# Performance work log

Measured on AMD Instinct MI355X. Metric: run time of the kernel, lower is better.

Reference implementation:

```python
import jax, jax.numpy as jnp
import numpy as np

E, B, D, T = 8, 4096, 2048, 2048
H = D // 2 + T // 2  # expert hidden dim = 2048
TOP_K = 2


def setup_inputs() -> dict:
    key = jax.random.key(0)
    ks = jax.random.split(key, 5)
    s_in = 1.0 / np.sqrt(D)
    s_h = 1.0 / np.sqrt(H)
    return {
        "xs": jax.random.normal(ks[0], (E, B, D), dtype=jnp.float32),
        "Wg": jax.random.normal(ks[1], (D,), dtype=jnp.float32) * s_in,
        "bg": jnp.zeros((1,), dtype=jnp.float32),
        "W1": jax.random.normal(ks[2], (E, D, H), dtype=jnp.float32) * s_in,
        "b1": jnp.zeros((E, H), dtype=jnp.float32),
        "W2": jax.random.normal(ks[3], (E, H, T), dtype=jnp.float32) * s_h,
        "b2": jnp.zeros((E, T), dtype=jnp.float32),
    }


def reference(xs, Wg, bg, W1, b1, W2, b2):
    # Gating: logits[b, e] = x[e][b] @ Wg + bg  -> [B, E]
    logits = jnp.einsum("ebd,d->be", xs, Wg) + bg
    probs = jax.nn.softmax(logits, axis=1)
    top_k_values, top_k_indices = jax.lax.top_k(probs, TOP_K)  # [B, K]

    # Dense expert compute over each expert's own input stream.
    # hidden[e, b, h] = relu(x[e] @ W1[e] + b1[e]); out[e, b, t] = hidden @ W2[e] + b2[e]
    hidden = jax.nn.relu(jnp.einsum("ebd,edh->ebh", xs, W1) + b1[:, None, :])
    expert_out = jnp.einsum("ebh,eht->ebt", hidden, W2) + b2[:, None, :]  # [E, B, T]

    # Gather the top-k experts per token. In the original, masked-dense compute
    # + output mask is mathematically identical to this gather.
    per_token = jnp.transpose(expert_out, (1, 0, 2))  # [B, E, T]
    selected = jnp.take_along_axis(per_token, top_k_indices[:, :, None], axis=1)  # [B, K, T]

    out = jnp.sum(top_k_values[:, :, None] * selected, axis=1)  # [B, T]
    return out, top_k_values
```

## Files before the change

### kernel.cpp

```cpp
#include <hip/hip_runtime.h>
#include <hip/hip_bf16.h>
#include <stdint.h>

#define E_ 8
#define B_ 4096
#define D_ 2048
#define T_ 2048
#define H_ 2048
#define KDIM 2048
#define NDIM 2048

typedef __attribute__((ext_vector_type(4))) float f32x4;
typedef __attribute__((ext_vector_type(4))) unsigned short u16x4;
typedef __attribute__((ext_vector_type(8))) unsigned short u16x8;
typedef __attribute__((ext_vector_type(8))) __bf16 bf16x8;

__device__ __forceinline__ unsigned short f2bf(float f) {
    __hip_bfloat16 h = __float2bfloat16(f);
    return __builtin_bit_cast(unsigned short, h);
}

__device__ __forceinline__ void gload_lds16(const void* g, void* lds) {
    __builtin_amdgcn_global_load_lds(
        (const __attribute__((address_space(1))) void*)g,
        (__attribute__((address_space(3))) void*)lds, 16, 0, 0);
}

__global__ __launch_bounds__(256) void moe_gating(
    const float* __restrict__ xs, const float* __restrict__ Wg,
    const float* __restrict__ bg, float* __restrict__ out_topk,
    float* __restrict__ prob_slot, int* __restrict__ counts,
    int* __restrict__ slot_of, unsigned short* __restrict__ A1)
{
    const int b = blockIdx.x;
    const int t = threadIdx.x;
    const int wave = t >> 6, lane = t & 63;
    __shared__ float red[E_][4];
    __shared__ int sh_i0, sh_i1;

    const f32x4 wg0 = ((const f32x4*)Wg)[t];
    const f32x4 wg1 = ((const f32x4*)Wg)[t + 256];

    f32x4 xa[E_], xb[E_];
    #pragma unroll
    for (int e = 0; e < E_; ++e) {
        const f32x4* xr = (const f32x4*)(xs + ((size_t)e * B_ + b) * D_);
        xa[e] = __builtin_nontemporal_load(&xr[t]);
        xb[e] = __builtin_nontemporal_load(&xr[t + 256]);
        float p = xa[e].x*wg0.x + xa[e].y*wg0.y + xa[e].z*wg0.z + xa[e].w*wg0.w
                + xb[e].x*wg1.x + xb[e].y*wg1.y + xb[e].z*wg1.z + xb[e].w*wg1.w;
        #pragma unroll
        for (int off = 32; off >= 1; off >>= 1) p += __shfl_xor(p, off);
        if (lane == 0) red[e][wave] = p;
    }
    __syncthreads();
    if (t == 0) {
        float pr[E_];
        float mx = -3.0e38f;
        #pragma unroll
        for (int e = 0; e < E_; ++e) {
            pr[e] = red[e][0] + red[e][1] + red[e][2] + red[e][3] + bg[0];
            mx = fmaxf(mx, pr[e]);
        }
        float s = 0.f;
        #pragma unroll
        for (int e = 0; e < E_; ++e) { pr[e] = expf(pr[e] - mx); s += pr[e]; }
        float inv = 1.0f / s;
        #pragma unroll
        for (int e = 0; e < E_; ++e) pr[e] *= inv;
        int i0 = 0;
        #pragma unroll
        for (int e = 1; e < E_; ++e) if (pr[e] > pr[i0]) i0 = e;
        int i1 = (i0 == 0) ? 1 : 0;
        #pragma unroll
        for (int e = 0; e < E_; ++e) { if (e != i0 && pr[e] > pr[i1]) i1 = e; }
        float p0 = pr[i0], p1 = pr[i1];
        out_topk[2*b]    = p0;
        out_topk[2*b+1]  = p1;
        prob_slot[2*b]   = p0;
        prob_slot[2*b+1] = p1;
        int pos0 = atomicAdd(&counts[i0], 1);
        slot_of[i0 * B_ + pos0] = 2*b;
        int pos1 = atomicAdd(&counts[i1], 1);
        slot_of[i1 * B_ + pos1] = 2*b + 1;
        sh_i0 = i0; sh_i1 = i1;
    }
    __syncthreads();
    const int i0 = sh_i0, i1 = sh_i1;
    f32x4 s0a = xa[0], s0b = xb[0], s1a = xa[0], s1b = xb[0];
    #pragma unroll
    for (int e = 0; e < E_; ++e) {
        if (i0 == e) { s0a = xa[e]; s0b = xb[e]; }
        if (i1 == e) { s1a = xa[e]; s1b = xb[e]; }
    }
    u16x4 w;
    w[0]=f2bf(s0a.x); w[1]=f2bf(s0a.y); w[2]=f2bf(s0a.z); w[3]=f2bf(s0a.w);
    ((u16x4*)(A1 + (size_t)(2*b) * D_))[t] = w;
    w[0]=f2bf(s0b.x); w[1]=f2bf(s0b.y); w[2]=f2bf(s0b.z); w[3]=f2bf(s0b.w);
    ((u16x4*)(A1 + (size_t)(2*b) * D_ + 1024))[t] = w;
    w[0]=f2bf(s1a.x); w[1]=f2bf(s1a.y); w[2]=f2bf(s1a.z); w[3]=f2bf(s1a.w);
    ((u16x4*)(A1 + (size_t)(2*b+1) * D_))[t] = w;
    w[0]=f2bf(s1b.x); w[1]=f2bf(s1b.y); w[2]=f2bf(s1b.z); w[3]=f2bf(s1b.w);
    ((u16x4*)(A1 + (size_t)(2*b+1) * D_ + 1024))[t] = w;
}

__global__ void build_tiles(const int* __restrict__ counts, int* __restrict__ tiles)
{
    if (threadIdx.x == 0 && blockIdx.x == 0) {
        int n = 0;
        for (int e = 0; e < E_; ++e) {
            int te = (counts[e] + 255) >> 8;
            for (int m = 0; m < te; ++m) tiles[1 + n++] = (e << 16) | m;
        }
        tiles[0] = n;
    }
}

template<int DUAL>
__global__ __launch_bounds__(256) void wtrans(
    const float* __restrict__ Wa, const float* __restrict__ Wb,
    unsigned short* __restrict__ Wta, unsigned short* __restrict__ Wtb)
{
    const int z  = blockIdx.z;
    const int e  = DUAL ? (z & 7) : z;
    const float* W = (DUAL && (z >> 3)) ? Wb : Wa;
    unsigned short* Wt = (DUAL && (z >> 3)) ? Wtb : Wta;
    const int kb = blockIdx.x * 64;
    const int nb = blockIdx.y * 64;
    const int t  = threadIdx.x;
    __shared__ float tile[64][68];

    const float* src = W + ((size_t)e * KDIM + kb) * NDIM + nb;
    {
        const int kr = t >> 2, nc = (t & 3) * 16;
        #pragma unroll
        for (int j = 0; j < 4; ++j) {
            f32x4 v = __builtin_nontemporal_load(
                (const f32x4*)(src + (size_t)kr * NDIM + nc + j * 4));
            *(f32x4*)&tile[kr][nc + j * 4] = v;
        }
    }
    __syncthreads();
    {
        const int nn = t >> 2, kc = (t & 3) * 16;
        unsigned short wbuf[16];
        #pragma unroll
        for (int j = 0; j < 16; ++j) wbuf[j] = f2bf(tile[kc + j][nn]);
        unsigned short* dst = Wt + ((size_t)e * NDIM + nb + nn) * KDIM + kb + kc;
        *(u16x8*)dst       = *(const u16x8*)&wbuf[0];
        *((u16x8*)dst + 1) = *(const u16x8*)&wbuf[8];
    }
}

#define BAR  __builtin_amdgcn_s_barrier()
#define PRIO1 __builtin_amdgcn_s_setprio(1)
#define PRIO0 __builtin_amdgcn_s_setprio(0)

template<int LAYER>
__global__ __launch_bounds__(1024, 4) void moe_gemm(
    const unsigned short* __restrict__ Abuf,
    const unsigned short* __restrict__ Wt,
    const float* __restrict__ bias,
    const int* __restrict__ counts,
    const int* __restrict__ tiles,
    const int* __restrict__ slot_of,
    const float* __restrict__ prob_slot,
    unsigned short* __restrict__ hidden_out,
    float* __restrict__ out)
{
    const int nMt = tiles[0];
    const int bid = blockIdx.x;
    const int mt  = bid >> 3;
    const int np  = bid & 7;
    if (mt >= nMt) return;
    const int info = tiles[1 + mt];
    const int e   = info >> 16;
    const int m0  = (info & 0xffff) * 256;
    const int n0  = np * 256;
    const int n_e = counts[e];

    const int t = threadIdx.x;
    const int lane = t & 63;
    const int w = t >> 6;
    const int wm = (w >> 2) * 64;
    const int wn = (w & 3) * 64;
    const int lg = lane >> 4;

    __shared__ u16x8 As[4 * 1024];
    __shared__ u16x8 Bs[4 * 1024];
    __shared__ int   slots_s[256];
    __shared__ float probs_s[256];

    if (t < 256) {
        int gm = m0 + t;
        int s = -1; float p = 0.f;
        if (gm < n_e) { s = slot_of[e * B_ + gm]; p = prob_slot[s]; }
        slots_s[t] = s; probs_s[t] = p;
    }
    __syncthreads();

    const int ksw = (((t & 3) ^ ((t >> 3) & 3)) << 3);
    const unsigned short* aptr;
    const unsigned short* bptr;
    {
        const int r = t >> 2;
        int s = slots_s[r]; if (s < 0) s = 0;
        aptr = Abuf + (size_t)s * KDIM + ksw;
        bptr = Wt + ((size_t)e * NDIM + n0 + r) * KDIM + ksw;
    }

#define STGA(BUF, KT) gload_lds16(aptr + (KT)*32, &As[(BUF)*1024 + w*64])
#define STGB(BUF, KT) gload_lds16(bptr + (KT)*32, &Bs[(BUF)*1024 + w*64])

    f32x4 acc[4][4];
    #pragma unroll
    for (int i = 0; i < 4; ++i)
        #pragma unroll
        for (int j = 0; j < 4; ++j) {
            f32x4 z = {0.f, 0.f, 0.f, 0.f};
            acc[i][j] = z;
        }

    STGA(0, 0); STGB(0, 0);
    STGA(1, 1); STGB(1, 1);
    STGA(2, 2); STGB(2, 2);

    const int usw = (lane >> 1) & 3;
    for (int kt = 0; kt < 64; ++kt) {
        asm volatile("s_waitcnt vmcnt(4)" ::: "memory");
        BAR;
        int tn = kt + 3; if (tn > 63) tn = 63;
        const int nb = (kt + 3) & 3;
        const int base = (kt & 3) * 1024;

        STGA(nb, tn);
        bf16x8 af[4];
        #pragma unroll
        for (int mi = 0; mi < 4; ++mi) {
            const int row = wm + mi * 16 + (lane & 15);
            af[mi] = __builtin_bit_cast(bf16x8, As[base + row * 4 + (lg ^ usw)]);
        }
        bf16x8 bq0, bq1;
        {
            const int r0 = wn + 0 * 16 + (lane & 15);
            const int r1 = wn + 1 * 16 + (lane & 15);
            bq0 = __builtin_bit_cast(bf16x8, Bs[base + r0 * 4 + (lg ^ usw)]);
            bq1 = __builtin_bit_cast(bf16x8, Bs[base + r1 * 4 + (lg ^ usw)]);
        }
        PRIO1;
        #pragma unroll
        for (int mi = 0; mi < 4; ++mi)
            acc[mi][0] = __builtin_amdgcn_mfma_f32_16x16x32_bf16(af[mi], bq0, acc[mi][0], 0, 0, 0);
        #pragma unroll
        for (int mi = 0; mi < 4; ++mi)
            acc[mi][1] = __builtin_amdgcn_mfma_f32_16x16x32_bf16(af[mi], bq1, acc[mi][1], 0, 0, 0);
        PRIO0;

        STGB(nb, tn);
        bf16x8 bq2, bq3;
        {
            const int r2 = wn + 2 * 16 + (lane & 15);
            const int r3 = wn + 3 * 16 + (lane & 15);
            bq2 = __builtin_bit_cast(bf16x8, Bs[base + r2 * 4 + (lg ^ usw)]);
            bq3 = __builtin_bit_cast(bf16x8, Bs[base + r3 * 4 + (lg ^ usw)]);
        }
        PRIO1;
        #pragma unroll
        for (int mi = 0; mi < 4; ++mi)
            acc[mi][2] = __builtin_amdgcn_mfma_f32_16x16x32_bf16(af[mi], bq2, acc[mi][2], 0, 0, 0);
        #pragma unroll
        for (int mi = 0; mi < 4; ++mi)
            acc[mi][3] = __builtin_amdgcn_mfma_f32_16x16x32_bf16(af[mi], bq3, acc[mi][3], 0, 0, 0);
        PRIO0;
    }
    asm volatile("s_waitcnt vmcnt(0)" ::: "memory");

    #pragma unroll
    for (int mi = 0; mi < 4; ++mi) {
        #pragma unroll
        for (int rr = 0; rr < 4; ++rr) {
            const int rloc = wm + mi * 16 + ((lane >> 4) << 2) + rr;
            const int s = slots_s[rloc];
            if (s < 0) continue;
            #pragma unroll
            for (int ni = 0; ni < 4; ++ni) {
                const int col = n0 + wn + ni * 16 + (lane & 15);
                float v = acc[mi][ni][rr];
                if (LAYER == 1) {
                    v += bias[e * NDIM + col];
                    v = fmaxf(v, 0.f);
                    hidden_out[(size_t)s * H_ + col] = f2bf(v);
                } else {
                    v = (v + bias[e * NDIM + col]) * probs_s[rloc];
                    atomicAdd(&out[(size_t)(s >> 1) * T_ + col], v);
                }
            }
        }
    }
#undef STGA
#undef STGB
}

extern "C" void kernel_launch(void* const* d_in, const int* in_sizes, int n_in,
                              void* d_out, int out_size, void* d_ws, size_t ws_size,
                              hipStream_t stream)
{
    const float* xs = (const float*)d_in[0];
    const float* Wg = (const float*)d_in[1];
    const float* bg = (const float*)d_in[2];
    const float* W1 = (const float*)d_in[3];
    const float* b1 = (const float*)d_in[4];
    const float* W2 = (const float*)d_in[5];
    const float* b2 = (const float*)d_in[6];

    float* out      = (float*)d_out;
    float* out_topk = out + (size_t)B_ * T_;

    char* ws = (char*)d_ws;
    int*   counts    = (int*)ws;
    int*   tiles     = (int*)(ws + 256);
    int*   slot_of   = (int*)(ws + 768);
    float* prob_slot = (float*)(ws + 768 + E_ * B_ * 4);
    size_t off = 768 + (size_t)E_ * B_ * 4 + 2 * B_ * 4;
    off = (off + 255) & ~(size_t)255;
    unsigned short* A1     = (unsigned short*)(ws + off); off += (size_t)2 * B_ * D_ * 2;
    unsigned short* hidden = (unsigned short*)(ws + off); off += (size_t)2 * B_ * H_ * 2;
    unsigned short* Wt1    = (unsigned short*)(ws + off); off += (size_t)E_ * KDIM * NDIM * 2;
    size_t off_big = off + (size_t)E_ * KDIM * NDIM * 2;
    unsigned short* Wt2 = (unsigned short*)(ws + off);

    const bool big = (ws_size >= off_big);

    hipMemsetAsync(counts, 0, 256, stream);
    hipMemsetAsync(out, 0, (size_t)B_ * T_ * sizeof(float), stream);

    dim3 blk(256), gblk(1024);
    dim3 ggrid(39 * 8);

    if (big) {
        dim3 tgrid(32, 32, 16);
        wtrans<1><<<tgrid, blk, 0, stream>>>(W1, W2, Wt1, Wt2);
        moe_gating<<<dim3(B_), dim3(256), 0, stream>>>(
            xs, Wg, bg, out_topk, prob_slot, counts, slot_of, A1);
        build_tiles<<<dim3(1), dim3(64), 0, stream>>>(counts, tiles);
        moe_gemm<1><<<ggrid, gblk, 0, stream>>>(
            A1, Wt1, b1, counts, tiles, slot_of, prob_slot, hidden, nullptr);
        moe_gemm<2><<<ggrid, gblk, 0, stream>>>(
            hidden, Wt2, b2, counts, tiles, slot_of, prob_slot, nullptr, out);
    } else {
        dim3 tgrid(32, 32, E_);
        moe_gating<<<dim3(B_), dim3(256), 0, stream>>>(
            xs, Wg, bg, out_topk, prob_slot, counts, slot_of, A1);
        build_tiles<<<dim3(1), dim3(64), 0, stream>>>(counts, tiles);
        wtrans<0><<<tgrid, blk, 0, stream>>>(W1, nullptr, Wt1, nullptr);
        moe_gemm<1><<<ggrid, gblk, 0, stream>>>(
            A1, Wt1, b1, counts, tiles, slot_of, prob_slot, hidden, nullptr);
        wtrans<0><<<tgrid, blk, 0, stream>>>(W2, nullptr, Wt1, nullptr);
        moe_gemm<2><<<ggrid, gblk, 0, stream>>>(
            hidden, Wt1, b2, counts, tiles, slot_of, prob_slot, nullptr, out);
    }
}
```

Before: 528.1 us.

## Shrink MoE GEMM M-tile to 128 rows with 512-thread blocks and triple buffering

Halves the GEMM M-tile from 256 to 128 rows, so each block uses 8 waves instead of 16, and grows the grid to cover the finer tiles. This cuts padding waste in each expert's last partial tile and gives more blocks for load balance across CUs. The pipeline goes from 4 LDS buffers with a prefetch depth of 3 to 3 rotating buffers with a depth of 2. The split staging and s_setprio hints are replaced by one combined stage and a single 4x4 MFMA block. In exchange, each B tile is reused by fewer rows, which raises weight traffic, and the shallower prefetch may expose more memory latency.

```diff
diff --git a/kernel.cpp b/kernel.cpp
--- a/kernel.cpp
+++ b/kernel.cpp
@@ -109,7 +109,7 @@
     if (threadIdx.x == 0 && blockIdx.x == 0) {
         int n = 0;
         for (int e = 0; e < E_; ++e) {
-            int te = (counts[e] + 255) >> 8;
+            int te = (counts[e] + 127) >> 7;
             for (int m = 0; m < te; ++m) tiles[1 + n++] = (e << 16) | m;
         }
         tiles[0] = n;
@@ -153,11 +153,9 @@
 }
 
 #define BAR  __builtin_amdgcn_s_barrier()
-#define PRIO1 __builtin_amdgcn_s_setprio(1)
-#define PRIO0 __builtin_amdgcn_s_setprio(0)
 
 template<int LAYER>
-__global__ __launch_bounds__(1024, 4) void moe_gemm(
+__global__ __launch_bounds__(512, 4) void moe_gemm(
     const unsigned short* __restrict__ Abuf,
     const unsigned short* __restrict__ Wt,
     const float* __restrict__ bias,
@@ -175,7 +173,7 @@
     if (mt >= nMt) return;
     const int info = tiles[1 + mt];
     const int e   = info >> 16;
-    const int m0  = (info & 0xffff) * 256;
+    const int m0  = (info & 0xffff) * 128;
     const int n0  = np * 256;
     const int n_e = counts[e];
 
@@ -186,12 +184,12 @@
     const int wn = (w & 3) * 64;
     const int lg = lane >> 4;
 
-    __shared__ u16x8 As[4 * 1024];
-    __shared__ u16x8 Bs[4 * 1024];
-    __shared__ int   slots_s[256];
-    __shared__ float probs_s[256];
-
-    if (t < 256) {
+    __shared__ u16x8 As[3 * 512];
+    __shared__ u16x8 Bs[3 * 1024];
+    __shared__ int   slots_s[128];
+    __shared__ float probs_s[128];
+
+    if (t < 128) {
         int gm = m0 + t;
         int s = -1; float p = 0.f;
         if (gm < n_e) { s = slot_of[e * B_ + gm]; p = prob_slot[s]; }
@@ -199,18 +197,24 @@
     }
     __syncthreads();
 
-    const int ksw = (((t & 3) ^ ((t >> 3) & 3)) << 3);
+    const int ksw = (((lane & 3) ^ ((lane >> 3) & 3)) << 3);
     const unsigned short* aptr;
-    const unsigned short* bptr;
     {
-        const int r = t >> 2;
+        const int r = w * 16 + (lane >> 2);
         int s = slots_s[r]; if (s < 0) s = 0;
         aptr = Abuf + (size_t)s * KDIM + ksw;
-        bptr = Wt + ((size_t)e * NDIM + n0 + r) * KDIM + ksw;
-    }
-
-#define STGA(BUF, KT) gload_lds16(aptr + (KT)*32, &As[(BUF)*1024 + w*64])
-#define STGB(BUF, KT) gload_lds16(bptr + (KT)*32, &Bs[(BUF)*1024 + w*64])
+    }
+    const unsigned short* bptr[2];
+    #pragma unroll
+    for (int j = 0; j < 2; ++j) {
+        const int r = w * 32 + j * 16 + (lane >> 2);
+        bptr[j] = Wt + ((size_t)e * NDIM + n0 + r) * KDIM + ksw;
+    }
+
+#define STG(BUF, KT) do{ \
+    gload_lds16(aptr + (KT)*32,    &As[(BUF)*512  + w*64]); \
+    gload_lds16(bptr[0] + (KT)*32, &Bs[(BUF)*1024 + w*128]); \
+    gload_lds16(bptr[1] + (KT)*32, &Bs[(BUF)*1024 + w*128 + 64]); }while(0)
 
     f32x4 acc[4][4];
     #pragma unroll
@@ -221,57 +225,39 @@
             acc[i][j] = z;
         }
 
-    STGA(0, 0); STGB(0, 0);
-    STGA(1, 1); STGB(1, 1);
-    STGA(2, 2); STGB(2, 2);
+    STG(0, 0); STG(1, 1);
 
     const int usw = (lane >> 1) & 3;
+    int c0 = 0;
+    int c2 = 2;
     for (int kt = 0; kt < 64; ++kt) {
-        asm volatile("s_waitcnt vmcnt(4)" ::: "memory");
+        asm volatile("s_waitcnt vmcnt(3)" ::: "memory");
         BAR;
-        int tn = kt + 3; if (tn > 63) tn = 63;
-        const int nb = (kt + 3) & 3;
-        const int base = (kt & 3) * 1024;
-
-        STGA(nb, tn);
-        bf16x8 af[4];
+        int tn = kt + 2; if (tn > 63) tn = 63;
+        STG(c2, tn);
+
+        const int baseA = c0 * 512;
+        const int baseB = c0 * 1024;
+        bf16x8 af[4], bq[4];
         #pragma unroll
         for (int mi = 0; mi < 4; ++mi) {
             const int row = wm + mi * 16 + (lane & 15);
-            af[mi] = __builtin_bit_cast(bf16x8, As[base + row * 4 + (lg ^ usw)]);
-        }
-        bf16x8 bq0, bq1;
-        {
-            const int r0 = wn + 0 * 16 + (lane & 15);
-            const int r1 = wn + 1 * 16 + (lane & 15);
-            bq0 = __builtin_bit_cast(bf16x8, Bs[base + r0 * 4 + (lg ^ usw)]);
-            bq1 = __builtin_bit_cast(bf16x8, Bs[base + r1 * 4 + (lg ^ usw)]);
-        }
-        PRIO1;
+            af[mi] = __builtin_bit_cast(bf16x8, As[baseA + row * 4 + (lg ^ usw)]);
+        }
+        #pragma unroll
+        for (int ni = 0; ni < 4; ++ni) {
+            const int row = wn + ni * 16 + (lane & 15);
+            bq[ni] = __builtin_bit_cast(bf16x8, Bs[baseB + row * 4 + (lg ^ usw)]);
+        }
         #pragma unroll
         for (int mi = 0; mi < 4; ++mi)
-            acc[mi][0] = __builtin_amdgcn_mfma_f32_16x16x32_bf16(af[mi], bq0, acc[mi][0], 0, 0, 0);
-        #pragma unroll
-        for (int mi = 0; mi < 4; ++mi)
-            acc[mi][1] = __builtin_amdgcn_mfma_f32_16x16x32_bf16(af[mi], bq1, acc[mi][1], 0, 0, 0);
-        PRIO0;
-
-        STGB(nb, tn);
-        bf16x8 bq2, bq3;
-        {
-            const int r2 = wn + 2 * 16 + (lane & 15);
-            const int r3 = wn + 3 * 16 + (lane & 15);
-            bq2 = __builtin_bit_cast(bf16x8, Bs[base + r2 * 4 + (lg ^ usw)]);
-            bq3 = __builtin_bit_cast(bf16x8, Bs[base + r3 * 4 + (lg ^ usw)]);
-        }
-        PRIO1;
-        #pragma unroll
-        for (int mi = 0; mi < 4; ++mi)
-            acc[mi][2] = __builtin_amdgcn_mfma_f32_16x16x32_bf16(af[mi], bq2, acc[mi][2], 0, 0, 0);
-        #pragma unroll
-        for (int mi = 0; mi < 4; ++mi)
-            acc[mi][3] = __builtin_amdgcn_mfma_f32_16x16x32_bf16(af[mi], bq3, acc[mi][3], 0, 0, 0);
-        PRIO0;
+            #pragma unroll
+            for (int ni = 0; ni < 4; ++ni)
+                acc[mi][ni] = __builtin_amdgcn_mfma_f32_16x16x32_bf16(
+                    af[mi], bq[ni], acc[mi][ni], 0, 0, 0);
+
+        c0 = (c0 == 2) ? 0 : c0 + 1;
+        c2 = (c2 == 2) ? 0 : c2 + 1;
     }
     asm volatile("s_waitcnt vmcnt(0)" ::: "memory");
 
@@ -297,8 +283,7 @@
             }
         }
     }
-#undef STGA
-#undef STGB
+#undef STG
 }
 
 extern "C" void kernel_launch(void* const* d_in, const int* in_sizes, int n_in,
@@ -334,8 +319,8 @@
     hipMemsetAsync(counts, 0, 256, stream);
     hipMemsetAsync(out, 0, (size_t)B_ * T_ * sizeof(float), stream);
 
-    dim3 blk(256), gblk(1024);
-    dim3 ggrid(39 * 8);
+    dim3 blk(256), gblk(512);
+    dim3 ggrid(72 * 8);
 
     if (big) {
         dim3 tgrid(32, 32, 16);
```

After: 542.8 us. +2.8%, slower.
